# Performance work log

Hardware: AMD Instinct MI355X
Metric: run time of the kernel (lower is better)

## Reference

```python
import jax, jax.numpy as jnp
import numpy as np

B, NT, NP = 4096, 2048, 1024
DT = 1e-3


def _cum_trap(y, dx):
    # cumulative trapezoid along last dim, zero-prepended (preserve_dims=True)
    c = jnp.cumsum((y[..., 1:] + y[..., :-1]) * (0.5 * dx), axis=-1)
    return jnp.concatenate([jnp.zeros_like(y[..., :1]), c], axis=-1)


def _trapz(y, dx):
    return jnp.sum(y[..., :-1] + y[..., 1:], axis=-1) * (0.5 * dx)


def _renorm(f, dx):
    # square-normalize so each trace integrates to 1 (valid pdf)
    sq = f * f
    return sq / _trapz(sq, dx)[..., None]


def _natural_cubic_coeffs(p, q):
    # p: [NP] uniform knots, q: [B, NP] values -> per-interval coeffs a,b,c,d [B, NP-1]
    h = p[1] - p[0]
    n = p.shape[0]
    rhs = 6.0 * (q[..., :-2] - 2.0 * q[..., 1:-1] + q[..., 2:]) / (h * h)  # [B, n-2]
    m = n - 2
    A = 4.0 * jnp.eye(m, dtype=q.dtype) + jnp.eye(m, k=1, dtype=q.dtype) + jnp.eye(m, k=-1, dtype=q.dtype)
    M_int = jnp.linalg.solve(A, rhs.T).T                      # [B, n-2]
    zero = jnp.zeros_like(q[..., :1])
    M = jnp.concatenate([zero, M_int, zero], axis=-1)          # natural BC: M0 = Mn = 0
    a = q[..., :-1]
    b = (q[..., 1:] - q[..., :-1]) / h - h * (2.0 * M[..., :-1] + M[..., 1:]) / 6.0
    c = M[..., :-1] / 2.0
    d = (M[..., 1:] - M[..., :-1]) / (6.0 * h)
    return a, b, c, d


def _spline_eval(p, coeffs, x):
    # evaluate batched natural cubic splines at x: [B, NT]
    a, b, c, d = coeffs
    idx = jnp.clip(jnp.searchsorted(p, x, side='right') - 1, 0, p.shape[0] - 2)  # [B, NT]
    s = x - p[idx]
    ag = jnp.take_along_axis(a, idx, axis=-1)
    bg = jnp.take_along_axis(b, idx, axis=-1)
    cg = jnp.take_along_axis(c, idx, axis=-1)
    dg = jnp.take_along_axis(d, idx, axis=-1)
    return ag + s * (bg + s * (cg + s * dg))


def setup_inputs() -> dict:
    key = jax.random.key(0)
    k1, k2 = jax.random.split(key)
    f = jax.random.normal(k1, (B, NT), dtype=jnp.float32)
    obs_data = jax.random.normal(k2, (B, NT), dtype=jnp.float32)
    t = jnp.arange(NT, dtype=jnp.float32) * DT
    p = jnp.linspace(0.0, 1.0, NP, dtype=jnp.float32)
    return {"f": f, "obs_data": obs_data, "t": t, "p": p}


def reference(f, obs_data, t, p):
    dt = t[1] - t[0]
    # ---- __init__: build per-trace quantile splines from obs_data ----
    obs_tilde = _renorm(obs_data, dt)                 # [B, NT] pdf
    cdf_obs = _cum_trap(obs_tilde, dt)                # [B, NT] cdf
    # true_quantile: step lookup q(p) = t[searchsorted(cdf, p)]
    idx = jax.vmap(lambda c: jnp.searchsorted(c, p))(cdf_obs)
    idx = jnp.clip(idx, 0, t.shape[0] - 1)
    q = t[idx]                                        # [B, NP]
    coeffs = _natural_cubic_coeffs(p, q)
    # ---- forward: W2 distance ----
    f_tilde = _renorm(f, dt)                          # [B, NT]
    F = _cum_trap(f_tilde, dt)                        # [B, NT] cdf of f
    off_diag = _spline_eval(p, coeffs, F)             # Q_obs(F(t)) [B, NT]
    diff = (t[None, :] - off_diag) ** 2
    integrated = _trapz(diff * f_tilde, dt)           # [B]
    return integrated.sum()
```

## Files before the change

kernel.cpp:

```cpp
#include <hip/hip_runtime.h>

#define NBATCH 4096
#define NT 2048
#define NP 1024
#define NTH 256
#define EPT 8
#define PPT 4
#define MSZ 1022
#define KT 4
#define IMGW 14

__device__ __forceinline__ int pI(int x) { return x + (x >> 3); }

__global__ __launch_bounds__(NTH, 8) void w2loss_kernel(
    const float* __restrict__ f,
    const float* __restrict__ obs,
    float* __restrict__ partial)
{
    __shared__ float sQp[1156];
    __shared__ float sMp[1156];
    __shared__ float sRp[MSZ + 2 * KT];
    __shared__ float sH[NTH];
    __shared__ float sPow[IMGW];
    __shared__ float sWSA[4], sWSB[4];
    __shared__ float sSqA[2], sSqB[2];
    __shared__ float sRed[4];

    const int tid  = threadIdx.x;
    const int lane = tid & 63;
    const int wid  = tid >> 6;
    const int b    = blockIdx.x;
    const int base = tid * EPT;

    const float dt      = 0.001f;
    const float half_dt = 0.0005f;
    const float h       = 0.00097751710654936461f;
    const float inv_h   = 1023.0f;
    const float inv_h2  = 1046529.0f;
    const float h6      = h * (1.0f / 6.0f);
    const float ih6     = inv_h * (1.0f / 6.0f);

    const float* orow = obs + (size_t)b * NT;
    const float* frow = f   + (size_t)b * NT;
    float4 o0 = *reinterpret_cast<const float4*>(orow + base);
    float4 o1 = *reinterpret_cast<const float4*>(orow + base + 4);
    float4 g0 = *reinterpret_cast<const float4*>(frow + base);
    float4 g1 = *reinterpret_cast<const float4*>(frow + base + 4);

    if (tid < IMGW) {
        const float rho = -0.26794919243112270f;
        float v = 1.0f;
        for (int i = 0; i < tid; ++i) v *= rho;
        sPow[tid] = v;
    }
    if (tid < KT) { sRp[tid] = 0.0f; sRp[KT + MSZ + tid] = 0.0f; }

    float prefA[EPT], prefB[EPT];
    {
        float s0;
        s0 = o0.x*o0.x; prefA[0] = s0;
        s0 = o0.y*o0.y; prefA[1] = prefA[0] + s0;
        s0 = o0.z*o0.z; prefA[2] = prefA[1] + s0;
        s0 = o0.w*o0.w; prefA[3] = prefA[2] + s0;
        s0 = o1.x*o1.x; prefA[4] = prefA[3] + s0;
        s0 = o1.y*o1.y; prefA[5] = prefA[4] + s0;
        s0 = o1.z*o1.z; prefA[6] = prefA[5] + s0;
        s0 = o1.w*o1.w; prefA[7] = prefA[6] + s0;
        s0 = g0.x*g0.x; prefB[0] = s0;
        s0 = g0.y*g0.y; prefB[1] = prefB[0] + s0;
        s0 = g0.z*g0.z; prefB[2] = prefB[1] + s0;
        s0 = g0.w*g0.w; prefB[3] = prefB[2] + s0;
        s0 = g1.x*g1.x; prefB[4] = prefB[3] + s0;
        s0 = g1.y*g1.y; prefB[5] = prefB[4] + s0;
        s0 = g1.z*g1.z; prefB[6] = prefB[5] + s0;
        s0 = g1.w*g1.w; prefB[7] = prefB[6] + s0;
    }
    float sqA7 = o1.w * o1.w;
    float sqB7 = g1.w * g1.w;
    sH[tid] = sqA7;

    float tsA = prefA[EPT - 1], tsB = prefB[EPT - 1];
    float wsA = tsA, wsB = tsB;
#pragma unroll
    for (int off = 1; off < 64; off <<= 1) {
        float uA = __shfl_up(wsA, off);
        float uB = __shfl_up(wsB, off);
        if (lane >= off) { wsA += uA; wsB += uB; }
    }
    if (lane == 63) { sWSA[wid] = wsA; sWSB[wid] = wsB; }
    if (tid == 0)       { sSqA[0] = prefA[0]; sSqB[0] = prefB[0]; }
    if (tid == NTH - 1) { sSqA[1] = sqA7;     sSqB[1] = sqB7; }
    __syncthreads();

    float exclA = wsA - tsA, exclB = wsB - tsB;
    if (wid > 0) { exclA += sWSA[0]; exclB += sWSB[0]; }
    if (wid > 1) { exclA += sWSA[1]; exclB += sWSB[1]; }
    if (wid > 2) { exclA += sWSA[2]; exclB += sWSB[2]; }
    float totA = sWSA[0] + sWSA[1] + sWSA[2] + sWSA[3];
    float totB = sWSB[0] + sWSB[1] + sWSB[2] + sWSB[3];
    float sq0A = sSqA[0], sq0B = sSqB[0];
    float invSA = 1.0f / (half_dt * (2.0f * totA - sSqA[1] - sq0A));
    float invSB = 1.0f / (half_dt * (2.0f * totB - sSqB[1] - sq0B));

    {
        float cm;
        if (tid == 0) cm = -1.0f;
        else {
            float sqprev = sH[tid - 1];
            cm = half_dt * (((exclA - sqprev) + exclA) - sq0A) * invSA;
        }
        float Pm = exclA;
#pragma unroll
        for (int e = 0; e < EPT; ++e) {
            int j = base + e;
            float Pj = exclA + prefA[e];
            float cc = (j == 0) ? 0.0f : half_dt * (Pm + Pj - sq0A) * invSA;
            int kLo = (int)floorf(cm * inv_h) + 1;
            int kHi = (int)floorf(cc * inv_h);
            if (kLo < 0) kLo = 0;
            if (j == NT - 1) kHi = NP - 1;
            else {
                if (e == EPT - 1) kHi += 1;
                if (kHi > NP - 1) kHi = NP - 1;
            }
            float qv = (float)j * dt;
            for (int k = kLo; k <= kHi; ++k) sQp[pI(k)] = qv;
            cm = cc;
            Pm = Pj;
        }
    }
    __syncthreads();

#pragma unroll
    for (int kk = 0; kk < PPT; ++kk) {
        int i = tid + kk * NTH;
        if (i < MSZ)
            sRp[KT + i] = 6.0f * (sQp[pI(i)] - 2.0f * sQp[pI(i + 1)] + sQp[pI(i + 2)]) * inv_h2;
    }
    __syncthreads();

    {
        const float Cg = 0.28867513459481288f;
        const float CP[KT + 1] = {
            1.0f, -0.26794919243112270f, 0.071796769724490830f,
            -0.019237886466840586f, 0.0051547761428899979f };
#pragma unroll
        for (int kk = 0; kk < PPT; ++kk) {
            int i = tid + kk * NTH;
            if (i < MSZ) {
                float acc = 0.0f;
#pragma unroll
                for (int d = -KT; d <= KT; ++d) {
                    int ad = d < 0 ? -d : d;
                    acc += CP[ad] * sRp[KT + i + d];
                }
                if (i + 1 < IMGW) {
                    float t1 = 0.0f;
#pragma unroll
                    for (int k2 = 0; k2 < IMGW - 1; ++k2) t1 += sPow[k2 + 1] * sRp[KT + k2];
                    acc -= sPow[i + 1] * t1;
                }
                if (MSZ - i < IMGW) {
                    float t2 = 0.0f;
#pragma unroll
                    for (int k2 = MSZ - IMGW + 1; k2 < MSZ; ++k2) t2 += sPow[MSZ - k2] * sRp[KT + k2];
                    acc -= sPow[MSZ - i] * t2;
                }
                sMp[pI(i + 1)] = Cg * acc;
            }
        }
    }
    if (tid == 0) { sMp[pI(0)] = 0.0f; sMp[pI(NP - 1)] = 0.0f; }
    __syncthreads();

    float local = 0.0f;
    float term0 = 0.0f, term7 = 0.0f;
    {
        const float c1B = half_dt * invSB;
        const float K0  = (2.0f * exclB - sq0B) * c1B;
        float tj = (float)base * dt;
#pragma unroll
        for (int e = 0; e < EPT; ++e) {
            float Gj = (e ? prefB[e - 1] : 0.0f) + prefB[e];
            float Fj = __builtin_fmaf(Gj, c1B, K0);
            float sqe = e ? (prefB[e] - prefB[e - 1]) : prefB[0];
            float kf = Fj * inv_h;
            kf = fminf(fmaxf(kf, 0.0f), 1022.0f);
            int k = (int)kf;
            float s = __builtin_fmaf(-h, (float)k, Fj);
            float q0 = sQp[pI(k)];
            float q1 = sQp[pI(k + 1)];
            float M0 = sMp[pI(k)];
            float M1 = sMp[pI(k + 1)];
            float bco = (q1 - q0) * inv_h - (2.0f * M0 + M1) * h6;
            float od  = q0 + s * (bco + s * (0.5f * M0 + s * (M1 - M0) * ih6));
            float dd  = tj - od;
            float term = dd * dd * sqe;
            local += term;
            if (e == 0) term0 = term;
            if (e == EPT - 1) term7 = term;
            tj += dt;
        }
    }
    if (tid == 0)       local -= 0.5f * term0;
    if (tid == NTH - 1) local -= 0.5f * term7;

#pragma unroll
    for (int off = 32; off > 0; off >>= 1) local += __shfl_down(local, off);
    if (lane == 0) sRed[wid] = local;
    __syncthreads();
    if (tid == 0) partial[b] = (sRed[0] + sRed[1] + sRed[2] + sRed[3]) * (dt * invSB);
}

__global__ __launch_bounds__(NTH) void w2loss_reduce(
    const float* __restrict__ partial, float* __restrict__ out)
{
    __shared__ float sRed[4];
    const int tid  = threadIdx.x;
    const int lane = tid & 63;
    const int wid  = tid >> 6;
    float s = 0.0f;
#pragma unroll
    for (int i = 0; i < 16; i += 4) {
        float4 v = *reinterpret_cast<const float4*>(partial + tid * 16 + i);
        s += v.x + v.y + v.z + v.w;
    }
#pragma unroll
    for (int off = 32; off > 0; off >>= 1) s += __shfl_down(s, off);
    if (lane == 0) sRed[wid] = s;
    __syncthreads();
    if (tid == 0) out[0] = sRed[0] + sRed[1] + sRed[2] + sRed[3];
}

extern "C" void kernel_launch(void* const* d_in, const int* in_sizes, int n_in,
                              void* d_out, int out_size, void* d_ws, size_t ws_size,
                              hipStream_t stream) {
    const float* f   = (const float*)d_in[0];
    const float* obs = (const float*)d_in[1];
    float* out     = (float*)d_out;
    float* partial = (float*)d_ws;

    w2loss_kernel<<<NBATCH, NTH, 0, stream>>>(f, obs, partial);
    w2loss_reduce<<<1, NTH, 0, stream>>>(partial, out);
}
```

Baseline: 30.71 us.

## Use 512-thread blocks, interleave Q and M in float2 LDS, single-wave reduce

```diff
diff --git a/kernel.cpp b/kernel.cpp
--- a/kernel.cpp
+++ b/kernel.cpp
@@ -3,28 +3,26 @@
 #define NBATCH 4096
 #define NT 2048
 #define NP 1024
-#define NTH 256
-#define EPT 8
-#define PPT 4
+#define NTH 512
+#define NW  (NTH / 64)
+#define EPT 4
+#define PPT 2
 #define MSZ 1022
 #define KT 4
 #define IMGW 14
-
-__device__ __forceinline__ int pI(int x) { return x + (x >> 3); }
 
 __global__ __launch_bounds__(NTH, 8) void w2loss_kernel(
     const float* __restrict__ f,
     const float* __restrict__ obs,
     float* __restrict__ partial)
 {
-    __shared__ float sQp[1156];
-    __shared__ float sMp[1156];
-    __shared__ float sRp[MSZ + 2 * KT];
-    __shared__ float sH[NTH];
-    __shared__ float sPow[IMGW];
-    __shared__ float sWSA[4], sWSB[4];
-    __shared__ float sSqA[2], sSqB[2];
-    __shared__ float sRed[4];
+    __shared__ float2 sQM[NP];
+    __shared__ float  sRp[MSZ + 2 * KT];
+    __shared__ float  sH[NTH];
+    __shared__ float  sPow[IMGW];
+    __shared__ float  sWSA[NW], sWSB[NW];
+    __shared__ float  sSqA[2], sSqB[2];
+    __shared__ float  sRed[NW];
 
     const int tid  = threadIdx.x;
     const int lane = tid & 63;
@@ -43,9 +41,7 @@
     const float* orow = obs + (size_t)b * NT;
     const float* frow = f   + (size_t)b * NT;
     float4 o0 = *reinterpret_cast<const float4*>(orow + base);
-    float4 o1 = *reinterpret_cast<const float4*>(orow + base + 4);
     float4 g0 = *reinterpret_cast<const float4*>(frow + base);
-    float4 g1 = *reinterpret_cast<const float4*>(frow + base + 4);
 
     if (tid < IMGW) {
         const float rho = -0.26794919243112270f;
@@ -56,28 +52,17 @@
     if (tid < KT) { sRp[tid] = 0.0f; sRp[KT + MSZ + tid] = 0.0f; }
 
     float prefA[EPT], prefB[EPT];
-    {
-        float s0;
-        s0 = o0.x*o0.x; prefA[0] = s0;
-        s0 = o0.y*o0.y; prefA[1] = prefA[0] + s0;
-        s0 = o0.z*o0.z; prefA[2] = prefA[1] + s0;
-        s0 = o0.w*o0.w; prefA[3] = prefA[2] + s0;
-        s0 = o1.x*o1.x; prefA[4] = prefA[3] + s0;
-        s0 = o1.y*o1.y; prefA[5] = prefA[4] + s0;
-        s0 = o1.z*o1.z; prefA[6] = prefA[5] + s0;
-        s0 = o1.w*o1.w; prefA[7] = prefA[6] + s0;
-        s0 = g0.x*g0.x; prefB[0] = s0;
-        s0 = g0.y*g0.y; prefB[1] = prefB[0] + s0;
-        s0 = g0.z*g0.z; prefB[2] = prefB[1] + s0;
-        s0 = g0.w*g0.w; prefB[3] = prefB[2] + s0;
-        s0 = g1.x*g1.x; prefB[4] = prefB[3] + s0;
-        s0 = g1.y*g1.y; prefB[5] = prefB[4] + s0;
-        s0 = g1.z*g1.z; prefB[6] = prefB[5] + s0;
-        s0 = g1.w*g1.w; prefB[7] = prefB[6] + s0;
-    }
-    float sqA7 = o1.w * o1.w;
-    float sqB7 = g1.w * g1.w;
-    sH[tid] = sqA7;
+    prefA[0] = o0.x*o0.x;
+    prefA[1] = prefA[0] + o0.y*o0.y;
+    prefA[2] = prefA[1] + o0.z*o0.z;
+    prefA[3] = prefA[2] + o0.w*o0.w;
+    prefB[0] = g0.x*g0.x;
+    prefB[1] = prefB[0] + g0.y*g0.y;
+    prefB[2] = prefB[1] + g0.z*g0.z;
+    prefB[3] = prefB[2] + g0.w*g0.w;
+    float sqAL = o0.w * o0.w;
+    float sqBL = g0.w * g0.w;
+    sH[tid] = sqAL;
 
     float tsA = prefA[EPT - 1], tsB = prefB[EPT - 1];
     float wsA = tsA, wsB = tsB;
@@ -89,15 +74,17 @@
     }
     if (lane == 63) { sWSA[wid] = wsA; sWSB[wid] = wsB; }
     if (tid == 0)       { sSqA[0] = prefA[0]; sSqB[0] = prefB[0]; }
-    if (tid == NTH - 1) { sSqA[1] = sqA7;     sSqB[1] = sqB7; }
+    if (tid == NTH - 1) { sSqA[1] = sqAL;     sSqB[1] = sqBL; }
     __syncthreads();
 
     float exclA = wsA - tsA, exclB = wsB - tsB;
-    if (wid > 0) { exclA += sWSA[0]; exclB += sWSB[0]; }
-    if (wid > 1) { exclA += sWSA[1]; exclB += sWSB[1]; }
-    if (wid > 2) { exclA += sWSA[2]; exclB += sWSB[2]; }
-    float totA = sWSA[0] + sWSA[1] + sWSA[2] + sWSA[3];
-    float totB = sWSB[0] + sWSB[1] + sWSB[2] + sWSB[3];
+    float totA = 0.0f, totB = 0.0f;
+#pragma unroll
+    for (int w = 0; w < NW; ++w) {
+        float a = sWSA[w], bv = sWSB[w];
+        if (w < wid) { exclA += a; exclB += bv; }
+        totA += a; totB += bv;
+    }
     float sq0A = sSqA[0], sq0B = sSqB[0];
     float invSA = 1.0f / (half_dt * (2.0f * totA - sSqA[1] - sq0A));
     float invSB = 1.0f / (half_dt * (2.0f * totB - sSqB[1] - sq0B));
@@ -124,7 +111,7 @@
                 if (kHi > NP - 1) kHi = NP - 1;
             }
             float qv = (float)j * dt;
-            for (int k = kLo; k <= kHi; ++k) sQp[pI(k)] = qv;
+            for (int k = kLo; k <= kHi; ++k) sQM[k].x = qv;
             cm = cc;
             Pm = Pj;
         }
@@ -135,7 +122,7 @@
     for (int kk = 0; kk < PPT; ++kk) {
         int i = tid + kk * NTH;
         if (i < MSZ)
-            sRp[KT + i] = 6.0f * (sQp[pI(i)] - 2.0f * sQp[pI(i + 1)] + sQp[pI(i + 2)]) * inv_h2;
+            sRp[KT + i] = 6.0f * (sQM[i].x - 2.0f * sQM[i + 1].x + sQM[i + 2].x) * inv_h2;
     }
     __syncthreads();
 
@@ -166,15 +153,15 @@
                     for (int k2 = MSZ - IMGW + 1; k2 < MSZ; ++k2) t2 += sPow[MSZ - k2] * sRp[KT + k2];
                     acc -= sPow[MSZ - i] * t2;
                 }
-                sMp[pI(i + 1)] = Cg * acc;
+                sQM[i + 1].y = Cg * acc;
             }
         }
     }
-    if (tid == 0) { sMp[pI(0)] = 0.0f; sMp[pI(NP - 1)] = 0.0f; }
+    if (tid == 0) { sQM[0].y = 0.0f; sQM[NP - 1].y = 0.0f; }
     __syncthreads();
 
     float local = 0.0f;
-    float term0 = 0.0f, term7 = 0.0f;
+    float term0 = 0.0f, termL = 0.0f;
     {
         const float c1B = half_dt * invSB;
         const float K0  = (2.0f * exclB - sq0B) * c1B;
@@ -188,48 +175,47 @@
             kf = fminf(fmaxf(kf, 0.0f), 1022.0f);
             int k = (int)kf;
             float s = __builtin_fmaf(-h, (float)k, Fj);
-            float q0 = sQp[pI(k)];
-            float q1 = sQp[pI(k + 1)];
-            float M0 = sMp[pI(k)];
-            float M1 = sMp[pI(k + 1)];
-            float bco = (q1 - q0) * inv_h - (2.0f * M0 + M1) * h6;
-            float od  = q0 + s * (bco + s * (0.5f * M0 + s * (M1 - M0) * ih6));
+            float2 qm0 = sQM[k];
+            float2 qm1 = sQM[k + 1];
+            float bco = (qm1.x - qm0.x) * inv_h - (2.0f * qm0.y + qm1.y) * h6;
+            float od  = qm0.x + s * (bco + s * (0.5f * qm0.y + s * (qm1.y - qm0.y) * ih6));
             float dd  = tj - od;
             float term = dd * dd * sqe;
             local += term;
             if (e == 0) term0 = term;
-            if (e == EPT - 1) term7 = term;
+            if (e == EPT - 1) termL = term;
             tj += dt;
         }
     }
     if (tid == 0)       local -= 0.5f * term0;
-    if (tid == NTH - 1) local -= 0.5f * term7;
+    if (tid == NTH - 1) local -= 0.5f * termL;
 
 #pragma unroll
     for (int off = 32; off > 0; off >>= 1) local += __shfl_down(local, off);
     if (lane == 0) sRed[wid] = local;
     __syncthreads();
-    if (tid == 0) partial[b] = (sRed[0] + sRed[1] + sRed[2] + sRed[3]) * (dt * invSB);
+    if (tid == 0) {
+        float t = 0.0f;
+#pragma unroll
+        for (int w = 0; w < NW; ++w) t += sRed[w];
+        partial[b] = t * (dt * invSB);
+    }
 }
 
-__global__ __launch_bounds__(NTH) void w2loss_reduce(
+__global__ __launch_bounds__(64) void w2loss_reduce(
     const float* __restrict__ partial, float* __restrict__ out)
 {
-    __shared__ float sRed[4];
-    const int tid  = threadIdx.x;
-    const int lane = tid & 63;
-    const int wid  = tid >> 6;
+    const int lane = threadIdx.x;
+    const float4* p4 = reinterpret_cast<const float4*>(partial);
     float s = 0.0f;
 #pragma unroll
-    for (int i = 0; i < 16; i += 4) {
-        float4 v = *reinterpret_cast<const float4*>(partial + tid * 16 + i);
+    for (int i = 0; i < 16; ++i) {
+        float4 v = p4[lane * 16 + i];
         s += v.x + v.y + v.z + v.w;
     }
 #pragma unroll
     for (int off = 32; off > 0; off >>= 1) s += __shfl_down(s, off);
-    if (lane == 0) sRed[wid] = s;
-    __syncthreads();
-    if (tid == 0) out[0] = sRed[0] + sRed[1] + sRed[2] + sRed[3];
+    if (lane == 0) out[0] = s;
 }
 
 extern "C" void kernel_launch(void* const* d_in, const int* in_sizes, int n_in,
@@ -241,5 +227,5 @@
     float* partial = (float*)d_ws;
 
     w2loss_kernel<<<NBATCH, NTH, 0, stream>>>(f, obs, partial);
-    w2loss_reduce<<<1, NTH, 0, stream>>>(partial, out);
+    w2loss_reduce<<<1, 64, 0, stream>>>(partial, out);
 }
```

Result: slower. 31.89 us (+3.8%).
